# Kernel optimization log

Measured on AMD Instinct MI355X. Metric: run time of the kernel, lower is better.

Reference implementation:

```python
import jax, jax.numpy as jnp
import numpy as np

B, C, N = 8, 512, 2048
C8 = C // 8


def setup_inputs() -> dict:
    key = jax.random.key(0)
    kx, kq, kk, kv, kg = jax.random.split(key, 5)
    return {
        "x": jax.random.normal(kx, (B, C, N), dtype=jnp.float32),
        "Wq": jax.random.normal(kq, (C8, C), dtype=jnp.float32) * (1.0 / np.sqrt(C)),
        "Wk": jax.random.normal(kk, (C8, C), dtype=jnp.float32) * (1.0 / np.sqrt(C)),
        "Wv": jax.random.normal(kv, (C, C), dtype=jnp.float32) * (1.0 / np.sqrt(C)),
        # torch init is gamma=0.0; use a small random value so the attention
        # branch contributes to the output.
        "gamma": jax.random.uniform(kg, (1,), dtype=jnp.float32),
    }


def reference(x, Wq, Wk, Wv, gamma):
    # 1x1 convs == per-position linear maps over channels
    f = jnp.einsum("oc,bcn->bon", Wq, x)   # [B, C/8, N]
    g = jnp.einsum("oc,bcn->bon", Wk, x)   # [B, C/8, N]
    h = jnp.einsum("oc,bcn->bon", Wv, x)   # [B, C,   N]
    # scores[b,n,m] = sum_c f[b,c,n] * g[b,c,m]  (unscaled, as in source)
    scores = jnp.einsum("bcn,bcm->bnm", f, g)  # [B, N, N]
    # softmax over dim=1 (the query-position axis) — atypical but faithful
    beta = jax.nn.softmax(scores, axis=1)
    # o = gamma * h @ beta + x
    o = gamma[0] * jnp.einsum("bcn,bnm->bcm", h, beta) + x
    return o
```

## Files before the change

### kernel.cpp

```cpp
#include <hip/hip_runtime.h>
#include <hip/hip_bf16.h>
#include <math.h>

#define NB 8
#define NC 512
#define NN 2048

typedef unsigned short u16;
typedef __attribute__((ext_vector_type(8))) short short8;
typedef __attribute__((ext_vector_type(4))) float f32x4;

__device__ __forceinline__ float bf16_to_f32(u16 v) {
  union { unsigned int u; float f; } c; c.u = ((unsigned int)v) << 16; return c.f;
}
__device__ __forceinline__ u16 f32_to_bf16(float f) {
  __hip_bfloat16 h = __float2bfloat16(f);
  union { __hip_bfloat16 h; u16 u; } c; c.h = h; return c.u;
}
__device__ __forceinline__ void split2(float v, unsigned short& hi, unsigned short& lo) {
  hi = f32_to_bf16(v);
  lo = f32_to_bf16(v - bf16_to_f32(hi));
}

__device__ __forceinline__ void gl_lds16(const void* g, void* l) {
  __builtin_amdgcn_global_load_lds(
      (const __attribute__((address_space(1))) unsigned int*)g,
      (__attribute__((address_space(3))) unsigned int*)l, 16, 0, 0);
}

__device__ __forceinline__ void stage128x32(const u16* __restrict__ src, size_t row_base,
                                            int selems, int k0, u16* lds, int tid) {
#pragma unroll
  for (int s = 0; s < 2; ++s) {
    int flat = s * 4096 + tid * 16;
    int row = flat >> 6;
    int kb  = flat & 63;
    const char* g = (const char*)(src + (row_base + row) * (size_t)selems + k0) + kb;
    u16* l = lds + s * 2048 + (tid & ~63) * 8;
    gl_lds16(g, l);
  }
}

__global__ __launch_bounds__(256)
void wsplit_kernel(const float* __restrict__ Wq, const float* __restrict__ Wk,
                   const float* __restrict__ Wv, u16* __restrict__ Whi,
                   u16* __restrict__ Wlo) {
  int idx = (blockIdx.x * 256 + threadIdx.x) * 4;
  int r = idx >> 9, c = idx & 511;
  const float* src;
  if (r < 64)       src = Wq + (size_t)r * NC + c;
  else if (r < 128) src = Wk + (size_t)(r - 64) * NC + c;
  else              src = Wv + (size_t)(r - 128) * NC + c;
  float4 v = *(const float4*)src;
  ushort4 hi, lo;
  split2(v.x, hi.x, lo.x); split2(v.y, hi.y, lo.y);
  split2(v.z, hi.z, lo.z); split2(v.w, hi.w, lo.w);
  *(ushort4*)&Whi[idx] = hi;
  *(ushort4*)&Wlo[idx] = lo;
}

__global__ __launch_bounds__(256)
void xsplit_kernel(const float* __restrict__ x, u16* __restrict__ xThi,
                   u16* __restrict__ xTlo) {
  const int b = blockIdx.z, c0 = blockIdx.y * 64, n0 = blockIdx.x * 64;
  __shared__ float t[64][65];
  const int tid = threadIdx.x, tx = tid & 15, ty = tid >> 4;
#pragma unroll
  for (int r = 0; r < 4; ++r) {
    int c = r * 16 + ty;
    float4 v = *(const float4*)&x[((size_t)b * NC + c0 + c) * NN + n0 + tx * 4];
    t[c][tx * 4 + 0] = v.x; t[c][tx * 4 + 1] = v.y;
    t[c][tx * 4 + 2] = v.z; t[c][tx * 4 + 3] = v.w;
  }
  __syncthreads();
#pragma unroll
  for (int r = 0; r < 4; ++r) {
    int n = r * 16 + ty;
    ushort4 hi, lo;
    split2(t[tx * 4 + 0][n], hi.x, lo.x);
    split2(t[tx * 4 + 1][n], hi.y, lo.y);
    split2(t[tx * 4 + 2][n], hi.z, lo.z);
    split2(t[tx * 4 + 3][n], hi.w, lo.w);
    size_t off = ((size_t)b * NN + n0 + n) * NC + c0 + tx * 4;
    *(ushort4*)&xThi[off] = hi;
    *(ushort4*)&xTlo[off] = lo;
  }
}

__global__ __launch_bounds__(256)
void proj_mfma_kernel(const u16* __restrict__ xThi, const u16* __restrict__ xTlo,
                      const u16* __restrict__ Whi, const u16* __restrict__ Wlo,
                      u16* __restrict__ fgThi, u16* __restrict__ fgTlo,
                      u16* __restrict__ hw) {
  const int b  = blockIdx.z;
  const int n0 = blockIdx.x * 128;
  const int r0 = blockIdx.y * 128;
  const bool fg = (r0 == 0);

  __shared__ u16 Wh[2][128 * 32], Wl[2][128 * 32], Xh[2][128 * 32], Xl[2][128 * 32];

  const int tid = threadIdx.x, wave = tid >> 6, lane = tid & 63;
  const int quad = lane >> 4, l16 = lane & 15;
  const int wa = (wave >> 1) * 64, wb = (wave & 1) * 64;
  const size_t xrow = (size_t)b * NN + n0;

  f32x4 acc[4][4];
#pragma unroll
  for (int i = 0; i < 4; ++i)
#pragma unroll
    for (int j = 0; j < 4; ++j) acc[i][j] = (f32x4){0.f, 0.f, 0.f, 0.f};

  stage128x32(Whi, r0, NC, 0, Wh[0], tid);
  stage128x32(xThi, xrow, NC, 0, Xh[0], tid);
  if (fg) {
    stage128x32(Wlo, r0, NC, 0, Wl[0], tid);
    stage128x32(xTlo, xrow, NC, 0, Xl[0], tid);
  }

  const int KIT = NC / 32;
  for (int ki = 0; ki < KIT; ++ki) {
    __syncthreads();
    if (ki + 1 < KIT) {
      const int nb = (ki + 1) & 1, k1 = (ki + 1) * 32;
      stage128x32(Whi, r0, NC, k1, Wh[nb], tid);
      stage128x32(xThi, xrow, NC, k1, Xh[nb], tid);
      if (fg) {
        stage128x32(Wlo, r0, NC, k1, Wl[nb], tid);
        stage128x32(xTlo, xrow, NC, k1, Xl[nb], tid);
      }
    }
    const int cur = ki & 1;

    if (fg) {
      short8 ah[4], al[4], bh[4], bl[4];
#pragma unroll
      for (int i = 0; i < 4; ++i) {
        ah[i] = *(short8*)&Wh[cur][(wa + i * 16 + l16) * 32 + quad * 8];
        al[i] = *(short8*)&Wl[cur][(wa + i * 16 + l16) * 32 + quad * 8];
      }
#pragma unroll
      for (int j = 0; j < 4; ++j) {
        bh[j] = *(short8*)&Xh[cur][(wb + j * 16 + l16) * 32 + quad * 8];
        bl[j] = *(short8*)&Xl[cur][(wb + j * 16 + l16) * 32 + quad * 8];
      }
#pragma unroll
      for (int i = 0; i < 4; ++i)
#pragma unroll
        for (int j = 0; j < 4; ++j) {
          acc[i][j] = __builtin_amdgcn_mfma_f32_16x16x32_bf16(ah[i], bh[j], acc[i][j], 0, 0, 0);
          acc[i][j] = __builtin_amdgcn_mfma_f32_16x16x32_bf16(ah[i], bl[j], acc[i][j], 0, 0, 0);
          acc[i][j] = __builtin_amdgcn_mfma_f32_16x16x32_bf16(al[i], bh[j], acc[i][j], 0, 0, 0);
        }
    } else {
      short8 ah[4], bh[4];
#pragma unroll
      for (int i = 0; i < 4; ++i)
        ah[i] = *(short8*)&Xh[cur][(wa + i * 16 + l16) * 32 + quad * 8];
#pragma unroll
      for (int j = 0; j < 4; ++j)
        bh[j] = *(short8*)&Wh[cur][(wb + j * 16 + l16) * 32 + quad * 8];
#pragma unroll
      for (int i = 0; i < 4; ++i)
#pragma unroll
        for (int j = 0; j < 4; ++j)
          acc[i][j] = __builtin_amdgcn_mfma_f32_16x16x32_bf16(ah[i], bh[j], acc[i][j], 0, 0, 0);
    }
  }

  if (fg) {
#pragma unroll
    for (int i = 0; i < 4; ++i)
#pragma unroll
      for (int j = 0; j < 4; ++j) {
        int rb = wa + i * 16 + quad * 4;
        int n  = n0 + wb + j * 16 + l16;
        ushort4 hi, lo;
        split2(acc[i][j][0], hi.x, lo.x); split2(acc[i][j][1], hi.y, lo.y);
        split2(acc[i][j][2], hi.z, lo.z); split2(acc[i][j][3], hi.w, lo.w);
        size_t off = ((size_t)b * NN + n) * 128 + rb;
        *(ushort4*)&fgThi[off] = hi;
        *(ushort4*)&fgTlo[off] = lo;
      }
  } else {
#pragma unroll
    for (int i = 0; i < 4; ++i)
#pragma unroll
      for (int j = 0; j < 4; ++j) {
        int nb = n0 + wa + i * 16 + quad * 4;
        int c  = r0 - 128 + wb + j * 16 + l16;
        ushort4 hi;
        hi.x = f32_to_bf16(acc[i][j][0]); hi.y = f32_to_bf16(acc[i][j][1]);
        hi.z = f32_to_bf16(acc[i][j][2]); hi.w = f32_to_bf16(acc[i][j][3]);
        *(ushort4*)&hw[((size_t)b * NC + c) * NN + nb] = hi;
      }
  }
}

__global__ __launch_bounds__(512)
void attn_out_kernel(const u16* __restrict__ fgThi, const u16* __restrict__ fgTlo,
                     const u16* __restrict__ hw, const float* __restrict__ x,
                     const float* __restrict__ gamma, float* __restrict__ out) {
  const int s = blockIdx.x;
  const int xcd = s & 7;
  const int t = s >> 3;
  const int mt = t & 15;
  const int ci4 = t >> 4;
  const int combo = (ci4 << 3) | xcd;
  const int b = combo >> 2;
  const int ch = combo & 3;
  const int m0 = mt * 128;
  const int c0 = ch * 128;

  __shared__ u16 Fh[2][64 * 64], Fl[2][64 * 64];
  __shared__ u16 Hs[2][128 * 64];
  __shared__ u16 Ps[128 * 64];
  float* Dn = (float*)Ps;

  const int tid = threadIdx.x, wave = tid >> 6, lane = tid & 63;
  const int quad = lane >> 4, l16 = lane & 15;
  const int ws_n = (wave >> 2) * 32, ws_m = (wave & 3) * 32;
  const int wv_c = (wave >> 2) * 64, wv_m = (wave & 3) * 32;

  const size_t frow = (size_t)b * NN;
  const size_t hrow = (size_t)b * NC + c0;

  short8 gh[2][2], gl[2][2];
#pragma unroll
  for (int j = 0; j < 2; ++j)
#pragma unroll
    for (int k = 0; k < 2; ++k) {
      size_t o = (frow + m0 + ws_m + j * 16 + l16) * 128 + 64 + k * 32 + quad * 8;
      gh[j][k] = *(const short8*)&fgThi[o];
      gl[j][k] = *(const short8*)&fgTlo[o];
    }

  {
    int flat = tid * 16;
    int row = flat >> 7, chunk = (flat >> 4) & 7;
    int kb = ((chunk ^ (row & 7)) << 4);
    gl_lds16((const char*)(fgThi + (frow + row) * 128) + kb, Fh[0] + (tid & ~63) * 8);
    gl_lds16((const char*)(fgTlo + (frow + row) * 128) + kb, Fl[0] + (tid & ~63) * 8);
#pragma unroll
    for (int s2 = 0; s2 < 2; ++s2) {
      int f2 = s2 * 8192 + tid * 16;
      int r2 = f2 >> 7, c2 = (f2 >> 4) & 7;
      gl_lds16((const char*)(hw + (hrow + r2) * NN) + ((c2 ^ (r2 & 7)) << 4),
               Hs[0] + s2 * 4096 + (tid & ~63) * 8);
    }
  }
  __syncthreads();

  float dsum0 = 0.f, dsum1 = 0.f;
  f32x4 ao[4][2];
#pragma unroll
  for (int i = 0; i < 4; ++i)
#pragma unroll
    for (int j = 0; j < 2; ++j) ao[i][j] = (f32x4){0.f, 0.f, 0.f, 0.f};

  const int NT = NN / 64;
  for (int it = 0; it < NT; ++it) {
    const int cur = it & 1;
    if (it + 1 < NT) {
      const int n1 = (it + 1) * 64;
      int flat = tid * 16;
      int row = flat >> 7, chunk = (flat >> 4) & 7;
      int kb = ((chunk ^ (row & 7)) << 4);
      gl_lds16((const char*)(fgThi + (frow + n1 + row) * 128) + kb,
               Fh[cur ^ 1] + (tid & ~63) * 8);
      gl_lds16((const char*)(fgTlo + (frow + n1 + row) * 128) + kb,
               Fl[cur ^ 1] + (tid & ~63) * 8);
#pragma unroll
      for (int s2 = 0; s2 < 2; ++s2) {
        int f2 = s2 * 8192 + tid * 16;
        int r2 = f2 >> 7, c2 = (f2 >> 4) & 7;
        gl_lds16((const char*)(hw + (hrow + r2) * NN + n1) + ((c2 ^ (r2 & 7)) << 4),
                 Hs[cur ^ 1] + s2 * 4096 + (tid & ~63) * 8);
      }
    }

    f32x4 as[2][2];
#pragma unroll
    for (int i = 0; i < 2; ++i)
#pragma unroll
      for (int j = 0; j < 2; ++j) as[i][j] = (f32x4){0.f, 0.f, 0.f, 0.f};
#pragma unroll
    for (int k = 0; k < 2; ++k) {
      short8 fh[2], fl[2];
#pragma unroll
      for (int i = 0; i < 2; ++i) {
        int rr = ws_n + i * 16 + l16;
        int ci = (((k * 4 + quad) ^ (rr & 7)) << 3);
        fh[i] = *(short8*)&Fh[cur][rr * 64 + ci];
        fl[i] = *(short8*)&Fl[cur][rr * 64 + ci];
      }
#pragma unroll
      for (int i = 0; i < 2; ++i)
#pragma unroll
        for (int j = 0; j < 2; ++j) {
          as[i][j] = __builtin_amdgcn_mfma_f32_16x16x32_bf16(fh[i], gh[j][k], as[i][j], 0, 0, 0);
          as[i][j] = __builtin_amdgcn_mfma_f32_16x16x32_bf16(fh[i], gl[j][k], as[i][j], 0, 0, 0);
          as[i][j] = __builtin_amdgcn_mfma_f32_16x16x32_bf16(fl[i], gh[j][k], as[i][j], 0, 0, 0);
        }
    }

#pragma unroll
    for (int j = 0; j < 2; ++j) {
      int m = ws_m + j * 16 + l16;
#pragma unroll
      for (int i = 0; i < 2; ++i) {
        float e0 = __expf(as[i][j][0]);
        float e1 = __expf(as[i][j][1]);
        float e2 = __expf(as[i][j][2]);
        float e3 = __expf(as[i][j][3]);
        if (j == 0) dsum0 += (e0 + e1) + (e2 + e3);
        else        dsum1 += (e0 + e1) + (e2 + e3);
        ushort4 pk;
        pk.x = f32_to_bf16(e0); pk.y = f32_to_bf16(e1);
        pk.z = f32_to_bf16(e2); pk.w = f32_to_bf16(e3);
        int nb = ws_n * 2 + i * 32 + quad * 8;
        int chunk = nb >> 4;
        int off = (nb & 15) >> 1;
        *(ushort4*)&Ps[m * 64 + ((chunk ^ (m & 7)) << 3) + off] = pk;
      }
    }

    asm volatile("s_waitcnt lgkmcnt(0)" ::: "memory");
    __builtin_amdgcn_s_barrier();

#pragma unroll
    for (int k = 0; k < 2; ++k) {
      short8 hh[4], pb[2];
#pragma unroll
      for (int i = 0; i < 4; ++i) {
        int rr = wv_c + i * 16 + l16;
        hh[i] = *(short8*)&Hs[cur][rr * 64 + ((((k * 4 + quad)) ^ (rr & 7)) << 3)];
      }
#pragma unroll
      for (int j = 0; j < 2; ++j) {
        int rm = wv_m + j * 16 + l16;
        pb[j] = *(short8*)&Ps[rm * 64 + ((((k * 4 + quad)) ^ (rm & 7)) << 3)];
      }
#pragma unroll
      for (int i = 0; i < 4; ++i)
#pragma unroll
        for (int j = 0; j < 2; ++j)
          ao[i][j] = __builtin_amdgcn_mfma_f32_16x16x32_bf16(hh[i], pb[j], ao[i][j], 0, 0, 0);
    }

    __syncthreads();
  }

  dsum0 += __shfl_xor(dsum0, 16); dsum0 += __shfl_xor(dsum0, 32);
  dsum1 += __shfl_xor(dsum1, 16); dsum1 += __shfl_xor(dsum1, 32);
  if (tid < 128) Dn[tid] = 0.f;
  __syncthreads();
  if (quad == 0) {
    atomicAdd(&Dn[ws_m + l16], dsum0);
    atomicAdd(&Dn[ws_m + 16 + l16], dsum1);
  }
  __syncthreads();

  const float g = gamma[0];
  float invd[2];
#pragma unroll
  for (int j = 0; j < 2; ++j)
    invd[j] = g / Dn[wv_m + j * 16 + l16];

#pragma unroll
  for (int i = 0; i < 4; ++i) {
#pragma unroll
    for (int j = 0; j < 2; ++j) {
      const int c = c0 + wv_c + i * 16 + quad * 4;
      const int m = m0 + wv_m + j * 16 + l16;
#pragma unroll
      for (int r = 0; r < 4; ++r) {
        size_t off = ((size_t)b * NC + c + r) * NN + m;
        out[off] = fmaf(invd[j], ao[i][j][r], x[off]);
      }
    }
  }
}

extern "C" void kernel_launch(void* const* d_in, const int* in_sizes, int n_in,
                              void* d_out, int out_size, void* d_ws, size_t ws_size,
                              hipStream_t stream) {
  const float* x     = (const float*)d_in[0];
  const float* Wq    = (const float*)d_in[1];
  const float* Wk    = (const float*)d_in[2];
  const float* Wv    = (const float*)d_in[3];
  const float* gamma = (const float*)d_in[4];
  float* out = (float*)d_out;

  char* ws = (char*)d_ws;
  u16*   xThi  = (u16*)ws;
  u16*   xTlo  = (u16*)(ws + 16777216);
  u16*   Whi   = (u16*)(ws + 33554432);
  u16*   Wlo   = (u16*)(ws + 34209792);
  u16*   fgThi = (u16*)(ws + 67108864);
  u16*   fgTlo = (u16*)(ws + 71303168);
  u16*   hw    = (u16*)(ws + 75497472);

  wsplit_kernel<<<dim3(320), 256, 0, stream>>>(Wq, Wk, Wv, Whi, Wlo);
  xsplit_kernel<<<dim3(NN / 64, NC / 64, NB), 256, 0, stream>>>(x, xThi, xTlo);
  proj_mfma_kernel<<<dim3(NN / 128, 5, NB), 256, 0, stream>>>(
      xThi, xTlo, Whi, Wlo, fgThi, fgTlo, hw);
  attn_out_kernel<<<dim3(512), 512, 0, stream>>>(fgThi, fgTlo, hw, x, gamma, out);
}
```

Before: 211.2 us.

## Retile attention output to 256 channels x 64 positions with single-buffered H

Changes each block's tile from 128 channels x 128 query positions to 256 channels x 64 positions. The score computation (a three-pass split-bf16 MFMA) is now done once per 256 output channels instead of once per 128, halving the redundant score/exp work. H is single-buffered and loaded at the start of each iteration, overlapping the score phase, with vmcnt waits placed before the barrier. The kernel also adds a min-blocks-per-CU launch bound. In exchange, H loads are no longer prefetched a full iteration ahead, which risks exposed memory latency, and the grid now holds 512 blocks.

Result: faster. 200.9 us (-4.9%).

```diff
diff --git a/kernel.cpp b/kernel.cpp
--- a/kernel.cpp
+++ b/kernel.cpp
@@ -196,43 +196,41 @@
   }
 }
 
-__global__ __launch_bounds__(512)
+__global__ __launch_bounds__(512, 4)
 void attn_out_kernel(const u16* __restrict__ fgThi, const u16* __restrict__ fgTlo,
                      const u16* __restrict__ hw, const float* __restrict__ x,
                      const float* __restrict__ gamma, float* __restrict__ out) {
   const int s = blockIdx.x;
   const int xcd = s & 7;
   const int t = s >> 3;
-  const int mt = t & 15;
-  const int ci4 = t >> 4;
-  const int combo = (ci4 << 3) | xcd;
-  const int b = combo >> 2;
-  const int ch = combo & 3;
-  const int m0 = mt * 128;
-  const int c0 = ch * 128;
+  const int mt = t & 31;
+  const int hi6 = t >> 5;
+  const int combo = (hi6 << 3) | xcd;
+  const int b = combo >> 1;
+  const int ch = combo & 1;
+  const int m0 = mt * 64;
+  const int c0 = ch * 256;
 
   __shared__ u16 Fh[2][64 * 64], Fl[2][64 * 64];
-  __shared__ u16 Hs[2][128 * 64];
-  __shared__ u16 Ps[128 * 64];
+  __shared__ u16 Hs[256 * 64];
+  __shared__ u16 Ps[64 * 64];
   float* Dn = (float*)Ps;
 
   const int tid = threadIdx.x, wave = tid >> 6, lane = tid & 63;
   const int quad = lane >> 4, l16 = lane & 15;
-  const int ws_n = (wave >> 2) * 32, ws_m = (wave & 3) * 32;
-  const int wv_c = (wave >> 2) * 64, wv_m = (wave & 3) * 32;
+  const int ws_n = (wave >> 2) * 32, ws_m = (wave & 3) * 16;
+  const int wv_c = (wave >> 1) * 64, wv_m = (wave & 1) * 32;
 
   const size_t frow = (size_t)b * NN;
   const size_t hrow = (size_t)b * NC + c0;
 
-  short8 gh[2][2], gl[2][2];
-#pragma unroll
-  for (int j = 0; j < 2; ++j)
-#pragma unroll
-    for (int k = 0; k < 2; ++k) {
-      size_t o = (frow + m0 + ws_m + j * 16 + l16) * 128 + 64 + k * 32 + quad * 8;
-      gh[j][k] = *(const short8*)&fgThi[o];
-      gl[j][k] = *(const short8*)&fgTlo[o];
-    }
+  short8 gh[2], gl[2];
+#pragma unroll
+  for (int k = 0; k < 2; ++k) {
+    size_t o = (frow + m0 + ws_m + l16) * 128 + 64 + k * 32 + quad * 8;
+    gh[k] = *(const short8*)&fgThi[o];
+    gl[k] = *(const short8*)&fgTlo[o];
+  }
 
   {
     int flat = tid * 16;
@@ -241,16 +239,16 @@
     gl_lds16((const char*)(fgThi + (frow + row) * 128) + kb, Fh[0] + (tid & ~63) * 8);
     gl_lds16((const char*)(fgTlo + (frow + row) * 128) + kb, Fl[0] + (tid & ~63) * 8);
 #pragma unroll
-    for (int s2 = 0; s2 < 2; ++s2) {
+    for (int s2 = 0; s2 < 4; ++s2) {
       int f2 = s2 * 8192 + tid * 16;
       int r2 = f2 >> 7, c2 = (f2 >> 4) & 7;
       gl_lds16((const char*)(hw + (hrow + r2) * NN) + ((c2 ^ (r2 & 7)) << 4),
-               Hs[0] + s2 * 4096 + (tid & ~63) * 8);
+               Hs + s2 * 4096 + (tid & ~63) * 8);
     }
   }
   __syncthreads();
 
-  float dsum0 = 0.f, dsum1 = 0.f;
+  float dsum = 0.f;
   f32x4 ao[4][2];
 #pragma unroll
   for (int i = 0; i < 4; ++i)
@@ -260,6 +258,17 @@
   const int NT = NN / 64;
   for (int it = 0; it < NT; ++it) {
     const int cur = it & 1;
+
+    if (it > 0) {
+      const int n1 = it * 64;
+#pragma unroll
+      for (int s2 = 0; s2 < 4; ++s2) {
+        int f2 = s2 * 8192 + tid * 16;
+        int r2 = f2 >> 7, c2 = (f2 >> 4) & 7;
+        gl_lds16((const char*)(hw + (hrow + r2) * NN + n1) + ((c2 ^ (r2 & 7)) << 4),
+                 Hs + s2 * 4096 + (tid & ~63) * 8);
+      }
+    }
     if (it + 1 < NT) {
       const int n1 = (it + 1) * 64;
       int flat = tid * 16;
@@ -269,20 +278,11 @@
                Fh[cur ^ 1] + (tid & ~63) * 8);
       gl_lds16((const char*)(fgTlo + (frow + n1 + row) * 128) + kb,
                Fl[cur ^ 1] + (tid & ~63) * 8);
-#pragma unroll
-      for (int s2 = 0; s2 < 2; ++s2) {
-        int f2 = s2 * 8192 + tid * 16;
-        int r2 = f2 >> 7, c2 = (f2 >> 4) & 7;
-        gl_lds16((const char*)(hw + (hrow + r2) * NN + n1) + ((c2 ^ (r2 & 7)) << 4),
-                 Hs[cur ^ 1] + s2 * 4096 + (tid & ~63) * 8);
-      }
-    }
-
-    f32x4 as[2][2];
-#pragma unroll
-    for (int i = 0; i < 2; ++i)
-#pragma unroll
-      for (int j = 0; j < 2; ++j) as[i][j] = (f32x4){0.f, 0.f, 0.f, 0.f};
+    }
+
+    f32x4 as[2];
+#pragma unroll
+    for (int i = 0; i < 2; ++i) as[i] = (f32x4){0.f, 0.f, 0.f, 0.f};
 #pragma unroll
     for (int k = 0; k < 2; ++k) {
       short8 fh[2], fl[2];
@@ -294,26 +294,22 @@
         fl[i] = *(short8*)&Fl[cur][rr * 64 + ci];
       }
 #pragma unroll
-      for (int i = 0; i < 2; ++i)
-#pragma unroll
-        for (int j = 0; j < 2; ++j) {
-          as[i][j] = __builtin_amdgcn_mfma_f32_16x16x32_bf16(fh[i], gh[j][k], as[i][j], 0, 0, 0);
-          as[i][j] = __builtin_amdgcn_mfma_f32_16x16x32_bf16(fh[i], gl[j][k], as[i][j], 0, 0, 0);
-          as[i][j] = __builtin_amdgcn_mfma_f32_16x16x32_bf16(fl[i], gh[j][k], as[i][j], 0, 0, 0);
-        }
-    }
-
-#pragma unroll
-    for (int j = 0; j < 2; ++j) {
-      int m = ws_m + j * 16 + l16;
-#pragma unroll
       for (int i = 0; i < 2; ++i) {
-        float e0 = __expf(as[i][j][0]);
-        float e1 = __expf(as[i][j][1]);
-        float e2 = __expf(as[i][j][2]);
-        float e3 = __expf(as[i][j][3]);
-        if (j == 0) dsum0 += (e0 + e1) + (e2 + e3);
-        else        dsum1 += (e0 + e1) + (e2 + e3);
+        as[i] = __builtin_amdgcn_mfma_f32_16x16x32_bf16(fh[i], gh[k], as[i], 0, 0, 0);
+        as[i] = __builtin_amdgcn_mfma_f32_16x16x32_bf16(fh[i], gl[k], as[i], 0, 0, 0);
+        as[i] = __builtin_amdgcn_mfma_f32_16x16x32_bf16(fl[i], gh[k], as[i], 0, 0, 0);
+      }
+    }
+
+    {
+      int m = ws_m + l16;
+#pragma unroll
+      for (int i = 0; i < 2; ++i) {
+        float e0 = __expf(as[i][0]);
+        float e1 = __expf(as[i][1]);
+        float e2 = __expf(as[i][2]);
+        float e3 = __expf(as[i][3]);
+        dsum += (e0 + e1) + (e2 + e3);
         ushort4 pk;
         pk.x = f32_to_bf16(e0); pk.y = f32_to_bf16(e1);
         pk.z = f32_to_bf16(e2); pk.w = f32_to_bf16(e3);
@@ -324,6 +320,8 @@
       }
     }
 
+    if (it + 1 < NT) asm volatile("s_waitcnt vmcnt(2)" ::: "memory");
+    else             asm volatile("s_waitcnt vmcnt(0)" ::: "memory");
     asm volatile("s_waitcnt lgkmcnt(0)" ::: "memory");
     __builtin_amdgcn_s_barrier();
 
@@ -333,7 +331,7 @@
 #pragma unroll
       for (int i = 0; i < 4; ++i) {
         int rr = wv_c + i * 16 + l16;
-        hh[i] = *(short8*)&Hs[cur][rr * 64 + ((((k * 4 + quad)) ^ (rr & 7)) << 3)];
+        hh[i] = *(short8*)&Hs[rr * 64 + ((((k * 4 + quad)) ^ (rr & 7)) << 3)];
       }
 #pragma unroll
       for (int j = 0; j < 2; ++j) {
@@ -350,14 +348,11 @@
     __syncthreads();
   }
 
-  dsum0 += __shfl_xor(dsum0, 16); dsum0 += __shfl_xor(dsum0, 32);
-  dsum1 += __shfl_xor(dsum1, 16); dsum1 += __shfl_xor(dsum1, 32);
-  if (tid < 128) Dn[tid] = 0.f;
+  dsum += __shfl_xor(dsum, 16);
+  dsum += __shfl_xor(dsum, 32);
+  if (tid < 64) Dn[tid] = 0.f;
   __syncthreads();
-  if (quad == 0) {
-    atomicAdd(&Dn[ws_m + l16], dsum0);
-    atomicAdd(&Dn[ws_m + 16 + l16], dsum1);
-  }
+  if (quad == 0) atomicAdd(&Dn[ws_m + l16], dsum);
   __syncthreads();
 
   const float g = gamma[0];
```
